# Kernel optimization log

Measured on AMD Instinct MI355X. Metric: run time of the kernel, lower is better.

Reference implementation:

```python
import jax, jax.numpy as jnp
import numpy as np

N = 100000
E = 1600000
D = 128      # input_dim == hidden_dim
L = 3        # num_layers
EPS = 1e-5


def setup_inputs() -> dict:
    key = jax.random.key(0)
    ks = jax.random.split(key, 12)
    s = 1.0 / np.sqrt(D)
    return {
        "x": jax.random.normal(ks[0], (N, D), jnp.float32),
        "edge_index": jax.random.randint(ks[1], (2, E), 0, N, jnp.int32),
        "reranker_scores": jax.random.normal(ks[2], (N,), jnp.float32),
        # input residual projection
        "proj_w": jax.random.normal(ks[3], (D, D), jnp.float32) * s,
        "proj_b": jnp.zeros((D,), jnp.float32),
        # SAGEConv weights (lin_l: aggregated neighbors, with bias; lin_r: root, no bias)
        "lin_l_w": jax.random.normal(ks[4], (L, D, D), jnp.float32) * s,
        "lin_l_b": jnp.zeros((L, D), jnp.float32),
        "lin_r_w": jax.random.normal(ks[5], (L, D, D), jnp.float32) * s,
        # layer norm params
        "ln_g": jnp.ones((L, D), jnp.float32),
        "ln_b": jnp.zeros((L, D), jnp.float32),
        # score head
        "head_w": jax.random.normal(ks[6], (D,), jnp.float32) * s,
        "head_b": jnp.zeros((), jnp.float32),
        "alpha": jnp.asarray(0.65, jnp.float32),
    }


def _layer_norm(h, g, b):
    mu = jnp.mean(h, axis=-1, keepdims=True)
    var = jnp.mean(jnp.square(h - mu), axis=-1, keepdims=True)
    return (h - mu) * jax.lax.rsqrt(var + EPS) * g + b


def reference(x, edge_index, reranker_scores, proj_w, proj_b,
              lin_l_w, lin_l_b, lin_r_w, ln_g, ln_b, head_w, head_b, alpha):
    src, dst = edge_index[0], edge_index[1]
    # in-degree for mean aggregation (clamped to avoid div-by-zero)
    deg = jax.ops.segment_sum(jnp.ones((E,), x.dtype), dst, num_segments=N)
    inv_deg = (1.0 / jnp.maximum(deg, 1.0))[:, None]  # [N,1]

    residual = x @ proj_w.T + proj_b  # input_proj(x)
    h = x
    for i in range(L):
        # SAGEConv(mean): lin_l(mean_{j->i} h_j) + lin_r(h_i)
        agg = jax.ops.segment_sum(h[src], dst, num_segments=N) * inv_deg
        h_new = agg @ lin_l_w[i].T + lin_l_b[i] + h @ lin_r_w[i].T
        h_new = jax.nn.relu(h_new)
        h_new = _layer_norm(h_new, ln_g[i], ln_b[i])
        # dropout p=0.0 -> identity
        h_new = h_new + (residual if i == 0 else h)
        h = h_new
    gnn_scores = h @ head_w + head_b  # [N]
    a = jax.nn.sigmoid(alpha)
    return a * reranker_scores + (1.0 - a) * gnn_scores
```

## Files before the change

kernel.cpp:

```cpp
#include <hip/hip_runtime.h>
#include <math.h>

#define N_NODES 100000
#define N_EDGES 1600000
#define D 128
#define NBKT 391

#define PREP_WL 48
#define PREP_WR 48
#define PREP_PJ 16
#define PREP_X  12500
#define PREP_BC 391

typedef __attribute__((ext_vector_type(8))) short short8;
typedef __attribute__((ext_vector_type(4))) float floatx4;

__device__ __forceinline__ float bf2f(unsigned short u) {
    union { unsigned int i; float f; } v;
    v.i = ((unsigned int)u) << 16;
    return v.f;
}
__device__ __forceinline__ unsigned short f2bf(float f) {
    union { float f; unsigned int i; } v;
    v.f = f;
    unsigned int u = v.i;
    u += 0x7fffu + ((u >> 16) & 1u);
    return (unsigned short)(u >> 16);
}
__device__ __forceinline__ unsigned short f2h(float f) {
    union { _Float16 h; unsigned short u; } c;
    c.h = (_Float16)f;
    return c.u;
}
__device__ __forceinline__ float h2f(unsigned short u) {
    union { unsigned short u; _Float16 h; } c;
    c.u = u;
    return (float)c.h;
}

__device__ __forceinline__ void split8(const float* __restrict__ p, short8& hi, short8& lo) {
    float4 v0 = *(const float4*)p;
    float4 v1 = *(const float4*)(p + 4);
    float f[8] = {v0.x, v0.y, v0.z, v0.w, v1.x, v1.y, v1.z, v1.w};
#pragma unroll
    for (int i = 0; i < 8; ++i) {
        unsigned short h = f2bf(f[i]);
        hi[i] = (short)h;
        lo[i] = (short)f2bf(f[i] - bf2f(h));
    }
}

__device__ __forceinline__ void split8h(const unsigned short* __restrict__ p, short8& hi, short8& lo) {
    uint4 v = *(const uint4*)p;
    unsigned int w[4] = {v.x, v.y, v.z, v.w};
#pragma unroll
    for (int i = 0; i < 4; ++i) {
#pragma unroll
        for (int j = 0; j < 2; ++j) {
            float f = h2f((unsigned short)((w[i] >> (j * 16)) & 0xffffu));
            unsigned short h = f2bf(f);
            hi[i * 2 + j] = (short)h;
            lo[i * 2 + j] = (short)f2bf(f - bf2f(h));
        }
    }
}

typedef __attribute__((address_space(3))) unsigned short lds_us;
typedef __attribute__((address_space(1))) const unsigned short gl_us;

__device__ __forceinline__ void stageG(unsigned short* sWbuf,
                                       const unsigned short* __restrict__ W, int tid) {
#pragma unroll
    for (int i = 0; i < 4; ++i) {
        int e = tid + 512 * i;
        int ct = e >> 8;
        int ks = (e >> 6) & 3;
        int q = (e >> 4) & 3;
        int l = e & 15;
        const unsigned short* g = W + (size_t)(ct * 16 + l) * D + ks * 32 + q * 8;
        unsigned short* lp = sWbuf + (size_t)(i * 512 + (tid & ~63)) * 8;
        __builtin_amdgcn_global_load_lds((gl_us*)g, (lds_us*)lp, 16, 0, 0);
    }
}

template <bool DUAL>
__device__ __forceinline__ void computeP(const unsigned short* sWbuf, int lane,
                                         const short8* Ah, const short8* Al, floatx4* acc) {
#pragma unroll
    for (int ks = 0; ks < 4; ++ks)
#pragma unroll
        for (int ct = 0; ct < 8; ++ct) {
            short8 wf = *(const short8*)(sWbuf + ((ct * 4 + ks) * 64 + lane) * 8);
            acc[ct] = __builtin_amdgcn_mfma_f32_16x16x32_bf16(Ah[ks], wf, acc[ct], 0, 0, 0);
            if (DUAL)
                acc[ct] = __builtin_amdgcn_mfma_f32_16x16x32_bf16(Al[ks], wf, acc[ct], 0, 0, 0);
        }
}

__device__ __forceinline__ void cvt_split_body(const float* __restrict__ s,
                                               unsigned short* __restrict__ hi,
                                               unsigned short* __restrict__ lo,
                                               int lb, int n4, int tid) {
    int i = lb * 256 + tid;
    if (i < n4) {
        float4 v = ((const float4*)s)[i];
        float f[4] = {v.x, v.y, v.z, v.w};
        ushort4 h, l;
        unsigned short* hp = (unsigned short*)&h;
        unsigned short* lp = (unsigned short*)&l;
#pragma unroll
        for (int c = 0; c < 4; ++c) {
            unsigned short hh = f2bf(f[c]);
            hp[c] = hh;
            lp[c] = f2bf(f[c] - bf2f(hh));
        }
        ((ushort4*)hi)[i] = h;
        ((ushort4*)lo)[i] = l;
    }
}

__global__ __launch_bounds__(256) void k_prep(
    const float* __restrict__ WlAll, unsigned short* __restrict__ Wlh, unsigned short* __restrict__ Wll,
    const float* __restrict__ WrAll, unsigned short* __restrict__ Wrh, unsigned short* __restrict__ Wrl,
    const float* __restrict__ projW, unsigned short* __restrict__ pWh, unsigned short* __restrict__ pWl,
    const float* __restrict__ x, unsigned short* __restrict__ xf,
    const int* __restrict__ dst, int* __restrict__ bcnt) {
    __shared__ int h[NBKT];
    int tid = threadIdx.x;
    int b = blockIdx.x;
    if (b < PREP_WL) { cvt_split_body(WlAll, Wlh, Wll, b, 3 * D * D / 4, tid); return; }
    b -= PREP_WL;
    if (b < PREP_WR) { cvt_split_body(WrAll, Wrh, Wrl, b, 3 * D * D / 4, tid); return; }
    b -= PREP_WR;
    if (b < PREP_PJ) { cvt_split_body(projW, pWh, pWl, b, D * D / 4, tid); return; }
    b -= PREP_PJ;
    if (b < PREP_X) {
        int i = b * 256 + tid;
        if (i < N_NODES * D / 4) {
            float4 v = ((const float4*)x)[i];
            ushort4 o;
            o.x = f2h(v.x); o.y = f2h(v.y); o.z = f2h(v.z); o.w = f2h(v.w);
            ((ushort4*)xf)[i] = o;
        }
        return;
    }
    b -= PREP_X;
    for (int i = tid; i < NBKT; i += 256) h[i] = 0;
    __syncthreads();
    int e0 = b * 4096;
#pragma unroll
    for (int i = 0; i < 16; ++i) {
        int e = e0 + tid + i * 256;
        if (e < N_EDGES) atomicAdd(&h[dst[e] >> 8], 1);
    }
    __syncthreads();
    for (int i = tid; i < NBKT; i += 256) {
        int c = h[i];
        if (c) atomicAdd(&bcnt[i], c);
    }
}

__global__ void k_bscan(const int* __restrict__ bcnt, int* __restrict__ bbase,
                        int* __restrict__ bcur, int* __restrict__ offs) {
    __shared__ int tmp[512];
    int tid = threadIdx.x;
    int v = (tid < NBKT) ? bcnt[tid] : 0;
    tmp[tid] = v;
    __syncthreads();
    for (int off = 1; off < 512; off <<= 1) {
        int t = (tid >= off) ? tmp[tid - off] : 0;
        __syncthreads();
        if (tid >= off) tmp[tid] += t;
        __syncthreads();
    }
    int ex = tmp[tid] - v;
    if (tid < NBKT) {
        bbase[tid] = ex;
        bcur[tid] = ex;
    }
    if (tid == 0) {
        bbase[NBKT] = N_EDGES;
        offs[N_NODES] = N_EDGES;
    }
}

__global__ __launch_bounds__(256) void k_bucket(const int* __restrict__ src,
                                                const int* __restrict__ dst,
                                                int* __restrict__ bcur, uint2* __restrict__ pairs) {
    __shared__ int cnt[NBKT];
    __shared__ int off[NBKT];
    int tid = threadIdx.x;
    for (int i = tid; i < NBKT; i += 256) cnt[i] = 0;
    __syncthreads();
    int e0 = blockIdx.x * 4096;
    int mydst[16], mysrc[16];
#pragma unroll
    for (int i = 0; i < 16; ++i) {
        int e = e0 + tid + i * 256;
        int d = (e < N_EDGES) ? dst[e] : -1;
        mydst[i] = d;
        mysrc[i] = (e < N_EDGES) ? src[e] : 0;
        if (d >= 0) atomicAdd(&cnt[d >> 8], 1);
    }
    __syncthreads();
    for (int b = tid; b < NBKT; b += 256) {
        int c = cnt[b];
        off[b] = c ? atomicAdd(&bcur[b], c) : 0;
    }
    __syncthreads();
#pragma unroll
    for (int i = 0; i < 16; ++i) {
        int d = mydst[i];
        if (d >= 0) {
            int p = atomicAdd(&off[d >> 8], 1);
            pairs[p] = make_uint2((unsigned)mysrc[i], (unsigned)d);
        }
    }
}

__global__ __launch_bounds__(256) void k_build(const uint2* __restrict__ pairs,
                                               const int* __restrict__ bbase,
                                               int* __restrict__ offs, float* __restrict__ invd,
                                               int* __restrict__ csr_src) {
    __shared__ int cnt[256];
    __shared__ int scn[256];
    __shared__ int cur[256];
    int b = blockIdx.x, tid = threadIdx.x;
    int node0 = b << 8;
    int nn = N_NODES - node0; if (nn > 256) nn = 256;
    int beg = bbase[b], end = bbase[b + 1];

    cnt[tid] = 0;
    __syncthreads();
    for (int e = beg + tid; e < end; e += 256) atomicAdd(&cnt[pairs[e].y & 255u], 1);
    __syncthreads();
    int v = cnt[tid];
    scn[tid] = v;
    __syncthreads();
    for (int off = 1; off < 256; off <<= 1) {
        int t = (tid >= off) ? scn[tid - off] : 0;
        __syncthreads();
        if (tid >= off) scn[tid] += t;
        __syncthreads();
    }
    int start = beg + scn[tid] - v;
    if (tid < nn) {
        offs[node0 + tid] = start;
        invd[node0 + tid] = 1.0f / (float)(v > 1 ? v : 1);
    }
    cur[tid] = start;
    __syncthreads();
    for (int e = beg + tid; e < end; e += 256) {
        uint2 pr = pairs[e];
        int p = atomicAdd(&cur[pr.y & 255u], 1);
        csr_src[p] = (int)pr.x;
    }
}

__global__ void k_agg_f16(const unsigned short* __restrict__ hf, const int* __restrict__ offs,
                          const int* __restrict__ csr_src, const float* __restrict__ inv_deg,
                          unsigned short* __restrict__ aggh) {
    int gw = (blockIdx.x * 256 + threadIdx.x) >> 6;
    int lane = threadIdx.x & 63;
    int half = lane >> 5, l32 = lane & 31;
    int node = gw * 2 + half;
    int beg = offs[node], end = offs[node + 1];
    float a0 = 0.f, a1 = 0.f, a2 = 0.f, a3 = 0.f;
    int e = beg;
    for (; e + 7 < end; e += 8) {
        int ss[8];
#pragma unroll
        for (int i = 0; i < 8; ++i) ss[i] = csr_src[e + i];
        uint2 vv[8];
#pragma unroll
        for (int i = 0; i < 8; ++i)
            vv[i] = ((const uint2*)(hf + (size_t)ss[i] * D))[l32];
#pragma unroll
        for (int i = 0; i < 8; ++i) {
            a0 += h2f((unsigned short)(vv[i].x & 0xffffu));
            a1 += h2f((unsigned short)(vv[i].x >> 16));
            a2 += h2f((unsigned short)(vv[i].y & 0xffffu));
            a3 += h2f((unsigned short)(vv[i].y >> 16));
        }
    }
    for (; e + 3 < end; e += 4) {
        int ss[4];
#pragma unroll
        for (int i = 0; i < 4; ++i) ss[i] = csr_src[e + i];
        uint2 vv[4];
#pragma unroll
        for (int i = 0; i < 4; ++i)
            vv[i] = ((const uint2*)(hf + (size_t)ss[i] * D))[l32];
#pragma unroll
        for (int i = 0; i < 4; ++i) {
            a0 += h2f((unsigned short)(vv[i].x & 0xffffu));
            a1 += h2f((unsigned short)(vv[i].x >> 16));
            a2 += h2f((unsigned short)(vv[i].y & 0xffffu));
            a3 += h2f((unsigned short)(vv[i].y >> 16));
        }
    }
    for (; e < end; ++e) {
        int s = csr_src[e];
        uint2 v = ((const uint2*)(hf + (size_t)s * D))[l32];
        a0 += h2f((unsigned short)(v.x & 0xffffu));
        a1 += h2f((unsigned short)(v.x >> 16));
        a2 += h2f((unsigned short)(v.y & 0xffffu));
        a3 += h2f((unsigned short)(v.y >> 16));
    }
    float id = inv_deg[node];
    ushort4 o;
    o.x = f2h(a0 * id); o.y = f2h(a1 * id); o.z = f2h(a2 * id); o.w = f2h(a3 * id);
    ((ushort4*)(aggh + (size_t)node * D))[l32] = o;
}

template <int MODE>
__global__ __launch_bounds__(512) void k_layer(
    const unsigned short* __restrict__ aggh,
    const float* __restrict__ xinf,
    const unsigned short* __restrict__ hinh,
    const unsigned short* __restrict__ Wlh, const unsigned short* __restrict__ Wll,
    const unsigned short* __restrict__ Wrh, const unsigned short* __restrict__ Wrl,
    const unsigned short* __restrict__ pWh, const unsigned short* __restrict__ pWl,
    const float* __restrict__ projB,
    const float* __restrict__ lb, const float* __restrict__ g,
    const float* __restrict__ beta,
    unsigned short* __restrict__ houtf,
    const float* __restrict__ hw, const float* __restrict__ hb_bias,
    const float* __restrict__ rr, const float* __restrict__ alphap,
    float* __restrict__ outp) {
    __shared__ unsigned short sW[2][16384];

    int tid = threadIdx.x;
    int w = tid >> 6, lane = tid & 63;
    int quad = lane >> 4, l16 = lane & 15;
    int base = blockIdx.x * 128 + w * 16;

    int ar = base + l16; if (ar > N_NODES - 1) ar = N_NODES - 1;
    int koff = quad * 8;

    floatx4 z = {0.f, 0.f, 0.f, 0.f};
    floatx4 acc[8];
#pragma unroll
    for (int ct = 0; ct < 8; ++ct) acc[ct] = z;

    stageG(sW[0], Wlh, tid);
    short8 ah[4], al[4];
#pragma unroll
    for (int ks = 0; ks < 4; ++ks) split8h(aggh + (size_t)ar * D + ks * 32 + koff, ah[ks], al[ks]);
    __syncthreads();

    stageG(sW[1], Wll, tid);
    computeP<true>(sW[0], lane, ah, al, acc);
    __syncthreads();

    stageG(sW[0], Wrh, tid);
    short8 bh[4], blo[4];
#pragma unroll
    for (int ks = 0; ks < 4; ++ks) {
        if (MODE == 0) split8(xinf + (size_t)ar * D + ks * 32 + koff, bh[ks], blo[ks]);
        else           split8h(hinh + (size_t)ar * D + ks * 32 + koff, bh[ks], blo[ks]);
    }
    computeP<false>(sW[1], lane, ah, al, acc);
    __syncthreads();

    stageG(sW[1], Wrl, tid);
    computeP<true>(sW[0], lane, bh, blo, acc);
    __syncthreads();

    if (MODE == 0) stageG(sW[0], pWh, tid);
    computeP<false>(sW[1], lane, bh, blo, acc);

    floatx4 accR[8];
    if (MODE == 0) {
#pragma unroll
        for (int ct = 0; ct < 8; ++ct) accR[ct] = z;
        __syncthreads();
        stageG(sW[1], pWl, tid);
        computeP<true>(sW[0], lane, bh, blo, accR);
        __syncthreads();
        computeP<false>(sW[1], lane, bh, blo, accR);
    }

    float lbv[8], gv[8], bv[8];
#pragma unroll
    for (int ct = 0; ct < 8; ++ct) {
        int n = ct * 16 + l16;
        lbv[ct] = lb[n];
        gv[ct] = g[n];
        bv[ct] = beta[n];
    }
#pragma unroll
    for (int ct = 0; ct < 8; ++ct)
#pragma unroll
        for (int r = 0; r < 4; ++r)
            acc[ct][r] = fmaxf(acc[ct][r] + lbv[ct], 0.f);

    float mu[4], rs[4];
#pragma unroll
    for (int r = 0; r < 4; ++r) {
        float s = 0.f, ss = 0.f;
#pragma unroll
        for (int ct = 0; ct < 8; ++ct) {
            float v = acc[ct][r];
            s += v;
            ss += v * v;
        }
#pragma unroll
        for (int m = 1; m < 16; m <<= 1) {
            s += __shfl_xor(s, m, 64);
            ss += __shfl_xor(ss, m, 64);
        }
        float m_ = s * (1.0f / 128.0f);
        float v_ = ss * (1.0f / 128.0f) - m_ * m_;
        mu[r] = m_;
        rs[r] = rsqrtf(v_ + 1e-5f);
    }

    float pbv[8], hwv[8];
    if (MODE == 0) {
#pragma unroll
        for (int ct = 0; ct < 8; ++ct) pbv[ct] = projB[ct * 16 + l16];
    }
    if (MODE == 2) {
#pragma unroll
        for (int ct = 0; ct < 8; ++ct) hwv[ct] = hw[ct * 16 + l16];
    }

#pragma unroll
    for (int r = 0; r < 4; ++r) {
        int crow = base + quad * 4 + r;
        bool valid = (crow < N_NODES);
        float m_ = mu[r], rs_ = rs[r];
        size_t ro = (size_t)crow * D;
        if (MODE == 2) {
            float s = 0.f;
#pragma unroll
            for (int ct = 0; ct < 8; ++ct) {
                int col = ct * 16 + l16;
                float sk = valid ? h2f(hinh[ro + col]) : 0.f;
                float o = (acc[ct][r] - m_) * rs_ * gv[ct] + bv[ct] + sk;
                s += o * hwv[ct];
            }
#pragma unroll
            for (int m = 1; m < 16; m <<= 1) s += __shfl_xor(s, m, 64);
            if (l16 == 0 && valid) {
                float a = 1.0f / (1.0f + expf(-alphap[0]));
                outp[crow] = a * rr[crow] + (1.0f - a) * (s + hb_bias[0]);
            }
        } else {
            if (!valid) continue;
#pragma unroll
            for (int ct = 0; ct < 8; ++ct) {
                int col = ct * 16 + l16;
                float sk = (MODE == 0) ? (accR[ct][r] + pbv[ct]) : h2f(hinh[ro + col]);
                float o = (acc[ct][r] - m_) * rs_ * gv[ct] + bv[ct] + sk;
                houtf[ro + col] = f2h(o);
            }
        }
    }
}

extern "C" void kernel_launch(void* const* d_in, const int* in_sizes, int n_in,
                              void* d_out, int out_size, void* d_ws, size_t ws_size,
                              hipStream_t stream) {
    const float* x     = (const float*)d_in[0];
    const int*   ei    = (const int*)d_in[1];
    const float* rr    = (const float*)d_in[2];
    const float* projW = (const float*)d_in[3];
    const float* projB = (const float*)d_in[4];
    const float* WlAll = (const float*)d_in[5];
    const float* lbAll = (const float*)d_in[6];
    const float* WrAll = (const float*)d_in[7];
    const float* gAll  = (const float*)d_in[8];
    const float* btAll = (const float*)d_in[9];
    const float* hw    = (const float*)d_in[10];
    const float* hbias = (const float*)d_in[11];
    const float* alpha = (const float*)d_in[12];
    float* out = (float*)d_out;

    char* p = (char*)d_ws;
    unsigned short* aggh = (unsigned short*)p; p += (size_t)N_NODES * D * 2;
    unsigned short* xf   = (unsigned short*)p; p += (size_t)N_NODES * D * 2;
    unsigned short* h0f  = (unsigned short*)p; p += (size_t)N_NODES * D * 2;
    unsigned short* h1f  = (unsigned short*)p; p += (size_t)N_NODES * D * 2;
    uint2* pairs = (uint2*)p; p += (size_t)N_EDGES * 8;
    unsigned short* Wlh = (unsigned short*)p; p += (size_t)3 * D * D * 2;
    unsigned short* Wll = (unsigned short*)p; p += (size_t)3 * D * D * 2;
    unsigned short* Wrh = (unsigned short*)p; p += (size_t)3 * D * D * 2;
    unsigned short* Wrl = (unsigned short*)p; p += (size_t)3 * D * D * 2;
    unsigned short* pWh = (unsigned short*)p; p += (size_t)D * D * 2;
    unsigned short* pWl = (unsigned short*)p; p += (size_t)D * D * 2;
    float* invd  = (float*)p; p += (size_t)N_NODES * 4;
    int* offs    = (int*)p; p += (size_t)(N_NODES + 2) * 4;
    int* csr_src = (int*)p; p += (size_t)N_EDGES * 4;
    int* bcnt    = (int*)p; p += 512 * 4;
    int* bbase   = (int*)p; p += 512 * 4;
    int* bcur    = (int*)p; p += 512 * 4;

    const int* src = ei;
    const int* dst = ei + N_EDGES;

    hipMemsetAsync(bcnt, 0, 512 * 4, stream);
    k_prep<<<PREP_WL + PREP_WR + PREP_PJ + PREP_X + PREP_BC, 256, 0, stream>>>(
        WlAll, Wlh, Wll, WrAll, Wrh, Wrl, projW, pWh, pWl, x, xf, dst, bcnt);
    k_bscan<<<1, 512, 0, stream>>>(bcnt, bbase, bcur, offs);
    k_bucket<<<NBKT, 256, 0, stream>>>(src, dst, bcur, pairs);
    k_build<<<NBKT, 256, 0, stream>>>(pairs, bbase, offs, invd, csr_src);

    int gl = (N_NODES + 127) / 128;
    int ga = N_NODES / 2 / 4;

    k_agg_f16<<<ga, 256, 0, stream>>>(xf, offs, csr_src, invd, aggh);
    k_layer<0><<<gl, 512, 0, stream>>>(aggh, x, nullptr,
                                       Wlh, Wll, Wrh, Wrl, pWh, pWl, projB,
                                       lbAll, gAll, btAll, h0f,
                                       nullptr, nullptr, nullptr, nullptr, nullptr);
    k_agg_f16<<<ga, 256, 0, stream>>>(h0f, offs, csr_src, invd, aggh);
    k_layer<1><<<gl, 512, 0, stream>>>(aggh, nullptr, h0f,
                                       Wlh + D * D, Wll + D * D, Wrh + D * D, Wrl + D * D,
                                       nullptr, nullptr, nullptr,
                                       lbAll + D, gAll + D, btAll + D, h1f,
                                       nullptr, nullptr, nullptr, nullptr, nullptr);
    k_agg_f16<<<ga, 256, 0, stream>>>(h1f, offs, csr_src, invd, aggh);
    k_layer<2><<<gl, 512, 0, stream>>>(aggh, nullptr, h1f,
                                       Wlh + 2 * D * D, Wll + 2 * D * D,
                                       Wrh + 2 * D * D, Wrl + 2 * D * D,
                                       nullptr, nullptr, nullptr,
                                       lbAll + 2 * D, gAll + 2 * D, btAll + 2 * D,
                                       nullptr,
                                       hw, hbias, rr, alpha, out);
}
```

Before: 508.5 us.

## Fuse CSR preprocessing stages into one cooperative kernel with grid syncs

```diff
diff --git a/kernel.cpp b/kernel.cpp
--- a/kernel.cpp
+++ b/kernel.cpp
@@ -1,16 +1,13 @@
 #include <hip/hip_runtime.h>
+#include <hip/hip_cooperative_groups.h>
 #include <math.h>
+
+namespace cg = cooperative_groups;
 
 #define N_NODES 100000
 #define N_EDGES 1600000
 #define D 128
 #define NBKT 391
-
-#define PREP_WL 48
-#define PREP_WR 48
-#define PREP_PJ 16
-#define PREP_X  12500
-#define PREP_BC 391
 
 typedef __attribute__((ext_vector_type(8))) short short8;
 typedef __attribute__((ext_vector_type(4))) float floatx4;
@@ -97,163 +94,152 @@
         }
 }
 
-__device__ __forceinline__ void cvt_split_body(const float* __restrict__ s,
-                                               unsigned short* __restrict__ hi,
-                                               unsigned short* __restrict__ lo,
-                                               int lb, int n4, int tid) {
-    int i = lb * 256 + tid;
-    if (i < n4) {
-        float4 v = ((const float4*)s)[i];
-        float f[4] = {v.x, v.y, v.z, v.w};
-        ushort4 h, l;
-        unsigned short* hp = (unsigned short*)&h;
-        unsigned short* lp = (unsigned short*)&l;
-#pragma unroll
-        for (int c = 0; c < 4; ++c) {
-            unsigned short hh = f2bf(f[c]);
-            hp[c] = hh;
-            lp[c] = f2bf(f[c] - bf2f(hh));
-        }
-        ((ushort4*)hi)[i] = h;
-        ((ushort4*)lo)[i] = l;
-    }
-}
-
-__global__ __launch_bounds__(256) void k_prep(
+__device__ __forceinline__ void cvt1(const float* __restrict__ s,
+                                     unsigned short* __restrict__ hi,
+                                     unsigned short* __restrict__ lo, int i) {
+    float4 v = ((const float4*)s)[i];
+    float f[4] = {v.x, v.y, v.z, v.w};
+    ushort4 h, l;
+    unsigned short* hp = (unsigned short*)&h;
+    unsigned short* lp = (unsigned short*)&l;
+#pragma unroll
+    for (int c = 0; c < 4; ++c) {
+        unsigned short hh = f2bf(f[c]);
+        hp[c] = hh;
+        lp[c] = f2bf(f[c] - bf2f(hh));
+    }
+    ((ushort4*)hi)[i] = h;
+    ((ushort4*)lo)[i] = l;
+}
+
+__global__ __launch_bounds__(512) void k_csr(
     const float* __restrict__ WlAll, unsigned short* __restrict__ Wlh, unsigned short* __restrict__ Wll,
     const float* __restrict__ WrAll, unsigned short* __restrict__ Wrh, unsigned short* __restrict__ Wrl,
     const float* __restrict__ projW, unsigned short* __restrict__ pWh, unsigned short* __restrict__ pWl,
     const float* __restrict__ x, unsigned short* __restrict__ xf,
-    const int* __restrict__ dst, int* __restrict__ bcnt) {
-    __shared__ int h[NBKT];
+    const int* __restrict__ src, const int* __restrict__ dst,
+    int* __restrict__ bcnt, int* __restrict__ bbase, int* __restrict__ bcur,
+    uint2* __restrict__ pairs, int* __restrict__ offs, float* __restrict__ invd,
+    int* __restrict__ csr_src) {
+    cg::grid_group grid = cg::this_grid();
+    __shared__ int sh[1024];
     int tid = threadIdx.x;
-    int b = blockIdx.x;
-    if (b < PREP_WL) { cvt_split_body(WlAll, Wlh, Wll, b, 3 * D * D / 4, tid); return; }
-    b -= PREP_WL;
-    if (b < PREP_WR) { cvt_split_body(WrAll, Wrh, Wrl, b, 3 * D * D / 4, tid); return; }
-    b -= PREP_WR;
-    if (b < PREP_PJ) { cvt_split_body(projW, pWh, pWl, b, D * D / 4, tid); return; }
-    b -= PREP_PJ;
-    if (b < PREP_X) {
-        int i = b * 256 + tid;
-        if (i < N_NODES * D / 4) {
-            float4 v = ((const float4*)x)[i];
-            ushort4 o;
-            o.x = f2h(v.x); o.y = f2h(v.y); o.z = f2h(v.z); o.w = f2h(v.w);
-            ((ushort4*)xf)[i] = o;
-        }
-        return;
-    }
-    b -= PREP_X;
-    for (int i = tid; i < NBKT; i += 256) h[i] = 0;
+    int nb = gridDim.x;
+    int gstr = nb * 512;
+
+    if (blockIdx.x == 0) bcnt[tid] = 0;
+    grid.sync();
+
+    for (int i = blockIdx.x * 512 + tid; i < 3 * D * D / 4; i += gstr) cvt1(WlAll, Wlh, Wll, i);
+    for (int i = blockIdx.x * 512 + tid; i < 3 * D * D / 4; i += gstr) cvt1(WrAll, Wrh, Wrl, i);
+    for (int i = blockIdx.x * 512 + tid; i < D * D / 4; i += gstr) cvt1(projW, pWh, pWl, i);
+    for (int i = blockIdx.x * 512 + tid; i < N_NODES * D / 4; i += gstr) {
+        float4 v = ((const float4*)x)[i];
+        ushort4 o;
+        o.x = f2h(v.x); o.y = f2h(v.y); o.z = f2h(v.z); o.w = f2h(v.w);
+        ((ushort4*)xf)[i] = o;
+    }
+    for (int i = tid; i < NBKT; i += 512) sh[i] = 0;
     __syncthreads();
-    int e0 = b * 4096;
-#pragma unroll
-    for (int i = 0; i < 16; ++i) {
-        int e = e0 + tid + i * 256;
-        if (e < N_EDGES) atomicAdd(&h[dst[e] >> 8], 1);
-    }
+    for (int e = blockIdx.x * 512 + tid; e < N_EDGES; e += gstr)
+        atomicAdd(&sh[dst[e] >> 8], 1);
     __syncthreads();
-    for (int i = tid; i < NBKT; i += 256) {
-        int c = h[i];
+    for (int i = tid; i < NBKT; i += 512) {
+        int c = sh[i];
         if (c) atomicAdd(&bcnt[i], c);
     }
-}
-
-__global__ void k_bscan(const int* __restrict__ bcnt, int* __restrict__ bbase,
-                        int* __restrict__ bcur, int* __restrict__ offs) {
-    __shared__ int tmp[512];
-    int tid = threadIdx.x;
-    int v = (tid < NBKT) ? bcnt[tid] : 0;
-    tmp[tid] = v;
-    __syncthreads();
-    for (int off = 1; off < 512; off <<= 1) {
-        int t = (tid >= off) ? tmp[tid - off] : 0;
-        __syncthreads();
-        if (tid >= off) tmp[tid] += t;
-        __syncthreads();
-    }
-    int ex = tmp[tid] - v;
-    if (tid < NBKT) {
-        bbase[tid] = ex;
-        bcur[tid] = ex;
-    }
-    if (tid == 0) {
-        bbase[NBKT] = N_EDGES;
-        offs[N_NODES] = N_EDGES;
-    }
-}
-
-__global__ __launch_bounds__(256) void k_bucket(const int* __restrict__ src,
-                                                const int* __restrict__ dst,
-                                                int* __restrict__ bcur, uint2* __restrict__ pairs) {
-    __shared__ int cnt[NBKT];
-    __shared__ int off[NBKT];
-    int tid = threadIdx.x;
-    for (int i = tid; i < NBKT; i += 256) cnt[i] = 0;
-    __syncthreads();
-    int e0 = blockIdx.x * 4096;
-    int mydst[16], mysrc[16];
-#pragma unroll
-    for (int i = 0; i < 16; ++i) {
-        int e = e0 + tid + i * 256;
-        int d = (e < N_EDGES) ? dst[e] : -1;
-        mydst[i] = d;
-        mysrc[i] = (e < N_EDGES) ? src[e] : 0;
-        if (d >= 0) atomicAdd(&cnt[d >> 8], 1);
-    }
-    __syncthreads();
-    for (int b = tid; b < NBKT; b += 256) {
-        int c = cnt[b];
-        off[b] = c ? atomicAdd(&bcur[b], c) : 0;
-    }
-    __syncthreads();
-#pragma unroll
-    for (int i = 0; i < 16; ++i) {
-        int d = mydst[i];
-        if (d >= 0) {
-            int p = atomicAdd(&off[d >> 8], 1);
-            pairs[p] = make_uint2((unsigned)mysrc[i], (unsigned)d);
-        }
-    }
-}
-
-__global__ __launch_bounds__(256) void k_build(const uint2* __restrict__ pairs,
-                                               const int* __restrict__ bbase,
-                                               int* __restrict__ offs, float* __restrict__ invd,
-                                               int* __restrict__ csr_src) {
-    __shared__ int cnt[256];
-    __shared__ int scn[256];
-    __shared__ int cur[256];
-    int b = blockIdx.x, tid = threadIdx.x;
-    int node0 = b << 8;
-    int nn = N_NODES - node0; if (nn > 256) nn = 256;
-    int beg = bbase[b], end = bbase[b + 1];
-
-    cnt[tid] = 0;
-    __syncthreads();
-    for (int e = beg + tid; e < end; e += 256) atomicAdd(&cnt[pairs[e].y & 255u], 1);
-    __syncthreads();
-    int v = cnt[tid];
-    scn[tid] = v;
-    __syncthreads();
-    for (int off = 1; off < 256; off <<= 1) {
-        int t = (tid >= off) ? scn[tid - off] : 0;
-        __syncthreads();
-        if (tid >= off) scn[tid] += t;
-        __syncthreads();
-    }
-    int start = beg + scn[tid] - v;
-    if (tid < nn) {
-        offs[node0 + tid] = start;
-        invd[node0 + tid] = 1.0f / (float)(v > 1 ? v : 1);
-    }
-    cur[tid] = start;
-    __syncthreads();
-    for (int e = beg + tid; e < end; e += 256) {
-        uint2 pr = pairs[e];
-        int p = atomicAdd(&cur[pr.y & 255u], 1);
-        csr_src[p] = (int)pr.x;
+    grid.sync();
+
+    if (blockIdx.x == 0) {
+        int v = (tid < NBKT) ? bcnt[tid] : 0;
+        sh[tid] = v;
+        __syncthreads();
+        for (int off = 1; off < 512; off <<= 1) {
+            int t = (tid >= off) ? sh[tid - off] : 0;
+            __syncthreads();
+            if (tid >= off) sh[tid] += t;
+            __syncthreads();
+        }
+        int ex = sh[tid] - v;
+        if (tid < NBKT) {
+            bbase[tid] = ex;
+            bcur[tid] = ex;
+        }
+        if (tid == 0) {
+            bbase[NBKT] = N_EDGES;
+            offs[N_NODES] = N_EDGES;
+        }
+    }
+    grid.sync();
+
+    {
+        int* cnt = sh;
+        int* off = sh + NBKT;
+        for (int i = tid; i < NBKT; i += 512) cnt[i] = 0;
+        __syncthreads();
+        int e0 = blockIdx.x * 4096;
+        int mydst[8], mysrc[8];
+#pragma unroll
+        for (int i = 0; i < 8; ++i) {
+            int e = e0 + tid + i * 512;
+            int d = (e < N_EDGES) ? dst[e] : -1;
+            mydst[i] = d;
+            mysrc[i] = (e < N_EDGES) ? src[e] : 0;
+            if (d >= 0) atomicAdd(&cnt[d >> 8], 1);
+        }
+        __syncthreads();
+        for (int b = tid; b < NBKT; b += 512) {
+            int c = cnt[b];
+            off[b] = c ? atomicAdd(&bcur[b], c) : 0;
+        }
+        __syncthreads();
+#pragma unroll
+        for (int i = 0; i < 8; ++i) {
+            int d = mydst[i];
+            if (d >= 0) {
+                int p = atomicAdd(&off[d >> 8], 1);
+                pairs[p] = make_uint2((unsigned)mysrc[i], (unsigned)d);
+            }
+        }
+    }
+    grid.sync();
+
+    {
+        int* cnt = sh;
+        int* scn = sh + 256;
+        int* cur = sh + 512;
+        int b = blockIdx.x;
+        int node0 = b << 8;
+        int nn = N_NODES - node0; if (nn > 256) nn = 256;
+        int beg = bbase[b], end = bbase[b + 1];
+
+        for (int i = tid; i < 256; i += 512) cnt[i] = 0;
+        __syncthreads();
+        for (int e = beg + tid; e < end; e += 512) atomicAdd(&cnt[pairs[e].y & 255u], 1);
+        __syncthreads();
+        int v = (tid < 256) ? cnt[tid] : 0;
+        if (tid < 256) scn[tid] = v;
+        __syncthreads();
+        for (int off = 1; off < 256; off <<= 1) {
+            int t = (tid >= off && tid < 256) ? scn[tid - off] : 0;
+            __syncthreads();
+            if (tid >= off && tid < 256) scn[tid] += t;
+            __syncthreads();
+        }
+        if (tid < 256) {
+            int start = beg + scn[tid] - v;
+            if (tid < nn) {
+                offs[node0 + tid] = start;
+                invd[node0 + tid] = 1.0f / (float)(v > 1 ? v : 1);
+            }
+            cur[tid] = start;
+        }
+        __syncthreads();
+        for (int e = beg + tid; e < end; e += 512) {
+            uint2 pr = pairs[e];
+            int p = atomicAdd(&cur[pr.y & 255u], 1);
+            csr_src[p] = (int)pr.x;
+        }
     }
 }
 
@@ -500,12 +486,18 @@
     const int* src = ei;
     const int* dst = ei + N_EDGES;
 
-    hipMemsetAsync(bcnt, 0, 512 * 4, stream);
-    k_prep<<<PREP_WL + PREP_WR + PREP_PJ + PREP_X + PREP_BC, 256, 0, stream>>>(
-        WlAll, Wlh, Wll, WrAll, Wrh, Wrl, projW, pWh, pWl, x, xf, dst, bcnt);
-    k_bscan<<<1, 512, 0, stream>>>(bcnt, bbase, bcur, offs);
-    k_bucket<<<NBKT, 256, 0, stream>>>(src, dst, bcur, pairs);
-    k_build<<<NBKT, 256, 0, stream>>>(pairs, bbase, offs, invd, csr_src);
+    {
+        void* args[] = {
+            (void*)&WlAll, (void*)&Wlh, (void*)&Wll,
+            (void*)&WrAll, (void*)&Wrh, (void*)&Wrl,
+            (void*)&projW, (void*)&pWh, (void*)&pWl,
+            (void*)&x, (void*)&xf,
+            (void*)&src, (void*)&dst,
+            (void*)&bcnt, (void*)&bbase, (void*)&bcur,
+            (void*)&pairs, (void*)&offs, (void*)&invd, (void*)&csr_src
+        };
+        hipLaunchCooperativeKernel((void*)k_csr, dim3(NBKT), dim3(512), args, 0, stream);
+    }
 
     int gl = (N_NODES + 127) / 128;
     int ga = N_NODES / 2 / 4;
```

After: 686.6 us. 35.0% more time.
